# Optimization experiments

Hardware: AMD Instinct MI355X
Metric: run time of the kernel (lower is better)

Reference implementation:

```python
import jax, jax.numpy as jnp
import numpy as np

NC, ND = 100000, 100000
E, L = 500000, 100000
HID, OUT = 128, 64
NH, HD = 4, 32
NL = 2


def setup_inputs() -> dict:
    key = jax.random.key(0)
    ks = jax.random.split(key, 16)
    f = jnp.float32
    s_lin = 1.0 / np.sqrt(HID)
    s_rel = 1.0 / np.sqrt(HD)
    return {
        "emb_C": jax.random.normal(ks[0], (NC, HID), f) * 0.1,
        "emb_D": jax.random.normal(ks[1], (ND, HID), f) * 0.1,
        "kW": jax.random.normal(ks[2], (NL, 2, HID, HID), f) * s_lin,
        "kb": jnp.zeros((NL, 2, HID), f),
        "qW": jax.random.normal(ks[3], (NL, 2, HID, HID), f) * s_lin,
        "qb": jnp.zeros((NL, 2, HID), f),
        "vW": jax.random.normal(ks[4], (NL, 2, HID, HID), f) * s_lin,
        "vb": jnp.zeros((NL, 2, HID), f),
        "aW": jax.random.normal(ks[5], (NL, 2, HID, HID), f) * s_lin,
        "ab": jnp.zeros((NL, 2, HID), f),
        "skip": jnp.ones((NL, 2), f),
        "arel": jax.random.normal(ks[6], (NL, 2, NH, HD, HD), f) * s_rel,
        "mrel": jax.random.normal(ks[7], (NL, 2, NH, HD, HD), f) * s_rel,
        "prel": jnp.ones((NL, 2, NH), f),
        "outW": jax.random.normal(ks[8], (2, HID, OUT), f) * s_lin,
        "outb": jnp.zeros((2, OUT), f),
        # edge_index for (Compound -> Disease) and reverse (Disease -> Compound)
        "ei_cd": jnp.stack([jax.random.randint(ks[9], (E,), 0, NC),
                            jax.random.randint(ks[10], (E,), 0, ND)]).astype(jnp.int32),
        "ei_dc": jnp.stack([jax.random.randint(ks[11], (E,), 0, ND),
                            jax.random.randint(ks[12], (E,), 0, NC)]).astype(jnp.int32),
        # edge_label_index: (Compound, Disease) pairs to score
        "eli": jnp.stack([jax.random.randint(ks[13], (L,), 0, NC),
                          jax.random.randint(ks[14], (L,), 0, ND)]).astype(jnp.int32),
    }


def _seg_softmax(a, seg, n):
    # numerically stable softmax over edges grouped by destination node
    amax = jax.ops.segment_max(a, seg, num_segments=n)
    amax = jnp.where(jnp.isfinite(amax), amax, 0.0)
    ex = jnp.exp(a - amax[seg])
    den = jax.ops.segment_sum(ex, seg, num_segments=n)
    return ex / (den[seg] + 1e-16)


def _hgt_layer(xs, p, ei_cd, ei_dc):
    kW, kb, qW, qb, vW, vb, aW, ab, skip, arel, mrel, prel = p
    # per-node-type K/Q/V projections, reshaped to [N, heads, head_dim]
    k = [(xs[t] @ kW[t] + kb[t]).reshape(-1, NH, HD) for t in range(2)]
    q = [(xs[t] @ qW[t] + qb[t]).reshape(-1, NH, HD) for t in range(2)]
    v = [(xs[t] @ vW[t] + vb[t]).reshape(-1, NH, HD) for t in range(2)]
    outs = [jnp.zeros_like(k[0]), jnp.zeros_like(k[1])]
    rels = [(0, 1, ei_cd), (1, 0, ei_dc)]  # (src_type, dst_type, edge_index)
    for r, (s, d, ei) in enumerate(rels):
        # relation-specific transforms applied per source node (as in PyG HGTConv)
        krel = jnp.einsum('nhd,hde->nhe', k[s], arel[r])
        vrel = jnp.einsum('nhd,hde->nhe', v[s], mrel[r])
        src, dst = ei[0], ei[1]
        ndst = xs[d].shape[0]
        a = (q[d][dst] * krel[src]).sum(-1) * prel[r] / np.sqrt(HD)  # [E, NH]
        alpha = _seg_softmax(a, dst, ndst)
        msg = vrel[src] * alpha[..., None]                           # [E, NH, HD]
        outs[d] = outs[d] + jax.ops.segment_sum(msg, dst, num_segments=ndst)
    new = []
    for t in range(2):
        o = outs[t].reshape(-1, HID)
        o = jax.nn.gelu(o) @ aW[t] + ab[t]
        g = jax.nn.sigmoid(skip[t])
        new.append(g * o + (1.0 - g) * xs[t])  # skip connection (in==out dims)
    return new


def reference(emb_C, emb_D, kW, kb, qW, qb, vW, vb, aW, ab, skip, arel, mrel, prel,
              outW, outb, ei_cd, ei_dc, eli):
    xs = [emb_C, emb_D]
    for l in range(NL):
        p = (kW[l], kb[l], qW[l], qb[l], vW[l], vb[l], aW[l], ab[l],
             skip[l], arel[l], mrel[l], prel[l])
        xs = _hgt_layer(xs, p, ei_cd, ei_dc)
        xs = [jax.nn.relu(x) for x in xs]  # dropout(0.2) in eval mode -> identity
    zC = xs[0] @ outW[0] + outb[0]
    zD = xs[1] @ outW[1] + outb[1]
    logits = jnp.clip((zC[eli[0]] * zD[eli[1]]).sum(-1), -10.0, 10.0)
    return logits
```

## Files before the change

kernel.cpp:

```cpp
#include <hip/hip_runtime.h>
#include <math.h>

#define NC_   100000
#define ND_   100000
#define NN_   100000
#define E_CNT 500000
#define L_CNT 100000
#define NH_   4
#define HD_   32
#define WCAT_SZ (129 * 384)

typedef __attribute__((ext_vector_type(8))) short short8;
typedef __attribute__((ext_vector_type(4))) float floatx4;

__device__ __forceinline__ float gelu_f(float x) {
    const float c0 = 0.7978845608028654f;
    float x3 = x * x * x;
    return 0.5f * x * (1.0f + tanhf(c0 * (x + 0.044715f * x3)));
}

__device__ __forceinline__ unsigned short bf_rne(float x) {
    unsigned int u = __float_as_uint(x);
    u += 0x7fffu + ((u >> 16) & 1u);
    return (unsigned short)(u >> 16);
}
__device__ __forceinline__ float bf_to_f(unsigned short b) {
    return __uint_as_float(((unsigned int)b) << 16);
}

__global__ __launch_bounds__(256) void fill0_int(int* __restrict__ p, int n) {
    int i = blockIdx.x * 256 + threadIdx.x;
    if (i < n) p[i] = 0;
}

__global__ __launch_bounds__(256) void count_dst(const int* __restrict__ dstA,
                                                 const int* __restrict__ dstB,
                                                 int* __restrict__ cnt) {
    int r = blockIdx.y;
    const int* dst = r ? dstB : dstA;
    int e = blockIdx.x * 256 + threadIdx.x;
    if (e < E_CNT) atomicAdd(&cnt[r * NN_ + dst[e]], 1);
}

__global__ __launch_bounds__(256) void scan_a(const int* __restrict__ cnt,
                                              int* __restrict__ excl,
                                              int* __restrict__ partials) {
    __shared__ int sd[256];
    int r = blockIdx.y;
    cnt += r * NN_; excl += r * (NN_ + 1); partials += r * 128;
    int b = blockIdx.x, t = threadIdx.x;
    int base = b * 1024 + t * 4;
    int v0 = (base + 0 < NN_) ? cnt[base + 0] : 0;
    int v1 = (base + 1 < NN_) ? cnt[base + 1] : 0;
    int v2 = (base + 2 < NN_) ? cnt[base + 2] : 0;
    int v3 = (base + 3 < NN_) ? cnt[base + 3] : 0;
    int tsum = v0 + v1 + v2 + v3;
    sd[t] = tsum; __syncthreads();
    for (int off = 1; off < 256; off <<= 1) {
        int x = (t >= off) ? sd[t - off] : 0;
        __syncthreads();
        sd[t] += x;
        __syncthreads();
    }
    int excl_t = sd[t] - tsum;
    if (t == 255) partials[b] = sd[t];
    int q = excl_t;
    if (base + 0 < NN_) excl[base + 0] = q; q += v0;
    if (base + 1 < NN_) excl[base + 1] = q; q += v1;
    if (base + 2 < NN_) excl[base + 2] = q; q += v2;
    if (base + 3 < NN_) excl[base + 3] = q;
}

__global__ __launch_bounds__(128) void scan_b(int* __restrict__ partials) {
    __shared__ int sd[128];
    partials += blockIdx.x * 128;
    int t = threadIdx.x;
    int orig = (t < 98) ? partials[t] : 0;
    sd[t] = orig; __syncthreads();
    for (int off = 1; off < 128; off <<= 1) {
        int x = (t >= off) ? sd[t - off] : 0;
        __syncthreads();
        sd[t] += x;
        __syncthreads();
    }
    if (t < 98) partials[t] = sd[t] - orig;
}

__global__ __launch_bounds__(256) void scan_c(int* __restrict__ row_ptr,
                                              const int* __restrict__ partials,
                                              int* __restrict__ cursor) {
    int r = blockIdx.y;
    row_ptr += r * (NN_ + 1); partials += r * 128; cursor += r * NN_;
    int b = blockIdx.x, t = threadIdx.x;
    int base = b * 1024 + t * 4;
    int add = partials[b];
    #pragma unroll
    for (int j = 0; j < 4; j++) {
        int i = base + j;
        if (i < NN_) { int v = row_ptr[i] + add; row_ptr[i] = v; cursor[i] = v; }
    }
    if (b == 0 && t == 0) row_ptr[NN_] = E_CNT;
}

__global__ __launch_bounds__(256) void scatter_edges(const int* __restrict__ srcA,
                                                     const int* __restrict__ dstA,
                                                     const int* __restrict__ srcB,
                                                     const int* __restrict__ dstB,
                                                     int* __restrict__ cursor,
                                                     int* __restrict__ srcs) {
    int r = blockIdx.y;
    const int* src = r ? srcB : srcA;
    const int* dst = r ? dstB : dstA;
    cursor += r * NN_; srcs += r * E_CNT;
    int e = blockIdx.x * 256 + threadIdx.x;
    if (e >= E_CNT) return;
    int pos = atomicAdd(&cursor[dst[e]], 1);
    srcs[pos] = src[e];
}

__global__ void fuse_weights(const float* __restrict__ qW, const float* __restrict__ qb,
                             const float* __restrict__ kW, const float* __restrict__ kb,
                             const float* __restrict__ vW, const float* __restrict__ vb,
                             const float* __restrict__ arel, const float* __restrict__ mrel,
                             float* __restrict__ WcatAll)
{
    int i  = blockIdx.x;
    int t  = blockIdx.y;
    int lyr = blockIdx.z;
    int oc = threadIdx.x;
    int lt = lyr * 2 + t;
    float* Wcat = WcatAll + (size_t)lt * WCAT_SZ;
    float val;
    if (oc < 128) {
        val = (i < 128) ? qW[(size_t)(lt * 128 + i) * 128 + oc] : qb[lt * 128 + oc];
    } else {
        int which = (oc >= 256);
        int cc = oc - (which ? 256 : 128);
        int h = cc >> 5, e = cc & 31;
        const float* W = which ? vW : kW;
        const float* b = which ? vb : kb;
        const float* R = (which ? mrel : arel) + (size_t)(lt * NH_ + h) * HD_ * HD_ + e;
        float s = 0.f;
        if (i < 128) {
            const float* wrow = W + (size_t)(lt * 128 + i) * 128 + h * 32;
            #pragma unroll
            for (int d2 = 0; d2 < 32; d2++) s += wrow[d2] * R[d2 * 32];
        } else {
            const float* brow = b + lt * 128 + h * 32;
            #pragma unroll
            for (int d2 = 0; d2 < 32; d2++) s += brow[d2] * R[d2 * 32];
        }
        val = s;
    }
    Wcat[(size_t)((i < 128) ? i : 128) * 384 + oc] = val;
}

__global__ __launch_bounds__(128)
void split_w(const float* __restrict__ W, int ldw, int matStride,
             unsigned short* __restrict__ out, int N, int outMatStride)
{
    int n = blockIdx.x;
    int mat = blockIdx.y;
    int k = threadIdx.x;
    float x = W[(size_t)mat * matStride + (size_t)k * ldw + n];
    unsigned short b0 = bf_rne(x);
    float x1 = x - bf_to_f(b0);
    unsigned short b1 = bf_rne(x1);
    float x2 = x1 - bf_to_f(b1);
    unsigned short b2 = bf_rne(x2);
    int ps = N * 128;
    unsigned short* o = out + (size_t)mat * outMatStride + (size_t)n * 128 + k;
    o[0] = b0; o[ps] = b1; o[2 * ps] = b2;
}

template<int TN, int POST>
__global__ __launch_bounds__(256)
void gemm_mfma(const float* __restrict__ A, int lda,
               const unsigned short* __restrict__ Bs3, int pstride,
               const float* __restrict__ bias,
               float* __restrict__ C, int ldc, int M,
               const float* __restrict__ resid, const float* __restrict__ skipv,
               int ySplit,
               const float* __restrict__ A2, const unsigned short* __restrict__ Bs32,
               int pstride2, const float* __restrict__ bias2,
               float* __restrict__ C2, int ldc2)
{
    constexpr int CT = TN / 16;
    __shared__ unsigned short Asl[3 * 64 * 40];
    __shared__ unsigned short Bsl[3 * TN * 40];
    int by = blockIdx.y;
    if (ySplit >= 0 && by >= ySplit) {
        A = A2; Bs3 = Bs32; pstride = pstride2; bias = bias2; C = C2; ldc = ldc2;
        by -= ySplit;
    }
    int tid  = threadIdx.x;
    int wave = tid >> 6, lane = tid & 63;
    int quad = lane >> 4, l16 = lane & 15;
    int bm = blockIdx.x * 64;
    int bn = by * TN;

    floatx4 acc[CT];
    #pragma unroll
    for (int ct = 0; ct < CT; ct++) acc[ct] = (floatx4){0.f, 0.f, 0.f, 0.f};

    int sm = tid >> 2;
    int kq = (tid & 3) * 8;
    int arow = bm + sm;
    bool aval = arow < M;
    const float* ap = A + (size_t)arow * lda + kq;
    int sn = tid >> 1;
    int kh = (tid & 1) * 16;
    const unsigned short* bp = Bs3 + (size_t)(bn + sn) * 128 + kh;

    for (int ks = 0; ks < 128; ks += 32) {
        __syncthreads();
        float xv[8];
        if (aval) {
            *(float4*)&xv[0] = *(const float4*)(ap + ks);
            *(float4*)&xv[4] = *(const float4*)(ap + ks + 4);
        } else {
            #pragma unroll
            for (int i = 0; i < 8; i++) xv[i] = 0.f;
        }
        #pragma unroll
        for (int i = 0; i < 8; i += 2) {
            float xa = xv[i], xb = xv[i + 1];
            unsigned short a0 = bf_rne(xa); float ra = xa - bf_to_f(a0);
            unsigned short a1 = bf_rne(ra); float ra2 = ra - bf_to_f(a1);
            unsigned short a2 = bf_rne(ra2);
            unsigned short c0 = bf_rne(xb); float rb = xb - bf_to_f(c0);
            unsigned short c1 = bf_rne(rb); float rb2 = rb - bf_to_f(c1);
            unsigned short c2 = bf_rne(rb2);
            int idx = sm * 40 + kq + i;
            *(unsigned int*)&Asl[idx]            = (unsigned)a0 | ((unsigned)c0 << 16);
            *(unsigned int*)&Asl[2560 + idx]     = (unsigned)a1 | ((unsigned)c1 << 16);
            *(unsigned int*)&Asl[5120 + idx]     = (unsigned)a2 | ((unsigned)c2 << 16);
        }
        if (sn < TN) {
            #pragma unroll
            for (int p = 0; p < 3; p++) {
                uint4 v0 = *(const uint4*)(bp + (size_t)p * pstride + ks);
                uint4 v1 = *(const uint4*)(bp + (size_t)p * pstride + ks + 8);
                int bidx = p * (TN * 40) + sn * 40 + kh;
                *(uint4*)&Bsl[bidx]     = v0;
                *(uint4*)&Bsl[bidx + 8] = v1;
            }
        }
        __syncthreads();
        int am = wave * 16 + l16;
        short8 af0 = *(const short8*)&Asl[am * 40 + quad * 8];
        short8 af1 = *(const short8*)&Asl[2560 + am * 40 + quad * 8];
        short8 af2 = *(const short8*)&Asl[5120 + am * 40 + quad * 8];
        #pragma unroll
        for (int ct = 0; ct < CT; ct++) {
            int bnn = (ct * 16 + l16) * 40 + quad * 8;
            short8 bf0 = *(const short8*)&Bsl[bnn];
            short8 bf1 = *(const short8*)&Bsl[TN * 40 + bnn];
            short8 bf2 = *(const short8*)&Bsl[2 * TN * 40 + bnn];
            acc[ct] = __builtin_amdgcn_mfma_f32_16x16x32_bf16(af0, bf2, acc[ct], 0, 0, 0);
            acc[ct] = __builtin_amdgcn_mfma_f32_16x16x32_bf16(af1, bf1, acc[ct], 0, 0, 0);
            acc[ct] = __builtin_amdgcn_mfma_f32_16x16x32_bf16(af2, bf0, acc[ct], 0, 0, 0);
            acc[ct] = __builtin_amdgcn_mfma_f32_16x16x32_bf16(af0, bf1, acc[ct], 0, 0, 0);
            acc[ct] = __builtin_amdgcn_mfma_f32_16x16x32_bf16(af1, bf0, acc[ct], 0, 0, 0);
            acc[ct] = __builtin_amdgcn_mfma_f32_16x16x32_bf16(af0, bf0, acc[ct], 0, 0, 0);
        }
    }

    float g = 0.f, omg = 0.f;
    if (POST) { float sv = skipv[0]; g = 1.0f / (1.0f + expf(-sv)); omg = 1.0f - g; }
    #pragma unroll
    for (int ct = 0; ct < CT; ct++) {
        int col = bn + ct * 16 + l16;
        float bv = bias[col];
        #pragma unroll
        for (int i = 0; i < 4; i++) {
            int row = bm + wave * 16 + quad * 4 + i;
            if (row < M) {
                float v = acc[ct][i] + bv;
                if (POST) {
                    float r = resid[(size_t)row * ldc + col];
                    v = fmaxf(g * v + omg * r, 0.f);
                }
                C[(size_t)row * ldc + col] = v;
            }
        }
    }
}

__global__ __launch_bounds__(256)
void attn_gather(const int* __restrict__ row_ptr, const int* __restrict__ srcs,
                 float* __restrict__ qo, const float* __restrict__ kv,
                 const float* __restrict__ prel, int ndst)
{
    int wave = (blockIdx.x * 256 + threadIdx.x) >> 6;
    int lane = threadIdx.x & 63;
    if (wave >= ndst) return;
    int d = wave;
    int gl = lane & 15;
    int group = lane >> 4;
    int h = gl >> 2;
    float pr = prel[h] * 0.17677669529663687f;
    int beg = row_ptr[d], end = row_ptr[d + 1];
    const float* qrow = qo + (size_t)d * 128 + gl * 8;
    float4 q0 = *(const float4*)(qrow);
    float4 q1 = *(const float4*)(qrow + 4);
    float m = -1.0e30f, l = 0.f;
    float4 acc0 = make_float4(0.f,0.f,0.f,0.f), acc1 = acc0;
    int nt = (end - beg + 3) >> 2;
    for (int t = 0; t < nt; t++) {
        int i = beg + (t << 2) + group;
        if (i < end) {
            int s = srcs[i];
            const float* row = kv + (size_t)s * 256 + gl * 8;
            float4 k0 = *(const float4*)(row);
            float4 k1 = *(const float4*)(row + 4);
            float4 v0 = *(const float4*)(row + 128);
            float4 v1 = *(const float4*)(row + 132);
            float part = q0.x*k0.x + q0.y*k0.y + q0.z*k0.z + q0.w*k0.w
                       + q1.x*k1.x + q1.y*k1.y + q1.z*k1.z + q1.w*k1.w;
            part += __shfl_xor(part, 1);
            part += __shfl_xor(part, 2);
            float a = part * pr;
            float mn = fmaxf(m, a);
            float scale = expf(m - mn);
            float p = expf(a - mn);
            l = l * scale + p;
            acc0.x = acc0.x * scale + p * v0.x;
            acc0.y = acc0.y * scale + p * v0.y;
            acc0.z = acc0.z * scale + p * v0.z;
            acc0.w = acc0.w * scale + p * v0.w;
            acc1.x = acc1.x * scale + p * v1.x;
            acc1.y = acc1.y * scale + p * v1.y;
            acc1.z = acc1.z * scale + p * v1.z;
            acc1.w = acc1.w * scale + p * v1.w;
            m = mn;
        }
    }
    #pragma unroll
    for (int mask = 16; mask <= 32; mask <<= 1) {
        float m_o = __shfl_xor(m, mask);
        float l_o = __shfl_xor(l, mask);
        float4 a0o, a1o;
        a0o.x = __shfl_xor(acc0.x, mask); a0o.y = __shfl_xor(acc0.y, mask);
        a0o.z = __shfl_xor(acc0.z, mask); a0o.w = __shfl_xor(acc0.w, mask);
        a1o.x = __shfl_xor(acc1.x, mask); a1o.y = __shfl_xor(acc1.y, mask);
        a1o.z = __shfl_xor(acc1.z, mask); a1o.w = __shfl_xor(acc1.w, mask);
        float mn = fmaxf(m, m_o);
        float s0 = expf(m - mn), s1 = expf(m_o - mn);
        l = l * s0 + l_o * s1;
        acc0.x = acc0.x * s0 + a0o.x * s1; acc0.y = acc0.y * s0 + a0o.y * s1;
        acc0.z = acc0.z * s0 + a0o.z * s1; acc0.w = acc0.w * s0 + a0o.w * s1;
        acc1.x = acc1.x * s0 + a1o.x * s1; acc1.y = acc1.y * s0 + a1o.y * s1;
        acc1.z = acc1.z * s0 + a1o.z * s1; acc1.w = acc1.w * s0 + a1o.w * s1;
        m = mn;
    }
    float inv = (beg == end) ? 0.f : 1.f / (l + 1e-16f);
    if (group == 0) {
        float* orow = qo + (size_t)d * 128 + gl * 8;
        float4 o0, o1;
        o0.x = gelu_f(acc0.x * inv); o0.y = gelu_f(acc0.y * inv);
        o0.z = gelu_f(acc0.z * inv); o0.w = gelu_f(acc0.w * inv);
        o1.x = gelu_f(acc1.x * inv); o1.y = gelu_f(acc1.y * inv);
        o1.z = gelu_f(acc1.z * inv); o1.w = gelu_f(acc1.w * inv);
        *(float4*)(orow)     = o0;
        *(float4*)(orow + 4) = o1;
    }
}

__global__ __launch_bounds__(256)
void score_pairs(const int* __restrict__ ic, const int* __restrict__ id,
                 const float* __restrict__ zC, const float* __restrict__ zD,
                 float* __restrict__ out)
{
    int gid = blockIdx.x * 256 + threadIdx.x;
    int p = gid >> 4, lane = gid & 15;
    if (p >= L_CNT) return;
    int c = ic[p], d = id[p];
    float4 a = *(const float4*)(zC + (size_t)c * 64 + lane * 4);
    float4 b = *(const float4*)(zD + (size_t)d * 64 + lane * 4);
    float s = a.x * b.x + a.y * b.y + a.z * b.z + a.w * b.w;
    s += __shfl_down(s, 8, 16);
    s += __shfl_down(s, 4, 16);
    s += __shfl_down(s, 2, 16);
    s += __shfl_down(s, 1, 16);
    if (lane == 0) out[p] = fminf(10.0f, fmaxf(-10.0f, s));
}

extern "C" void kernel_launch(void* const* d_in, const int* in_sizes, int n_in,
                              void* d_out, int out_size, void* d_ws, size_t ws_size,
                              hipStream_t stream)
{
    float* xC = (float*)d_in[0];
    float* xD = (float*)d_in[1];
    const float* kW   = (const float*)d_in[2];
    const float* kb   = (const float*)d_in[3];
    const float* qW   = (const float*)d_in[4];
    const float* qb   = (const float*)d_in[5];
    const float* vW   = (const float*)d_in[6];
    const float* vb   = (const float*)d_in[7];
    const float* aW   = (const float*)d_in[8];
    const float* ab   = (const float*)d_in[9];
    const float* skip = (const float*)d_in[10];
    const float* arel = (const float*)d_in[11];
    const float* mrel = (const float*)d_in[12];
    const float* prel = (const float*)d_in[13];
    const float* outW = (const float*)d_in[14];
    const float* outb = (const float*)d_in[15];
    const int* ei_cd  = (const int*)d_in[16];
    const int* ei_dc  = (const int*)d_in[17];
    const int* eli    = (const int*)d_in[18];

    float* ws = (float*)d_ws;
    size_t off = 0;
    float* kv    = ws + off; off += (size_t)NN_ * 256;
    float* qo    = ws + off; off += (size_t)NN_ * 128;
    float* Wcat  = ws + off; off += (size_t)4 * WCAT_SZ;
    unsigned short* WsCat = (unsigned short*)(ws + off); off += (4 * 3 * 384 * 128) / 2;
    unsigned short* aWs   = (unsigned short*)(ws + off); off += (4 * 3 * 128 * 128) / 2;
    unsigned short* outWs = (unsigned short*)(ws + off); off += (2 * 3 * 64 * 128) / 2;
    int* iws = (int*)(ws + off);
    size_t ioff = 0;
    int* rp      = iws + ioff; ioff += 2 * (NN_ + 1);
    int* srcsA   = iws + ioff; ioff += 2 * E_CNT;
    int* cnt     = iws + ioff; ioff += 2 * NN_;
    int* cursor  = iws + ioff; ioff += 2 * NN_;
    int* partial = iws + ioff; ioff += 256;
    float* zC = kv;
    float* zD = kv + (size_t)NN_ * 128;

    const int gridM = (NN_ + 63) / 64;
    const int gE    = (E_CNT + 255) / 256;
    const int gN2   = (2 * NN_ + 255) / 256;
    const int gScan = 98;
    const int gGath = (NN_ + 3) / 4;

    fill0_int<<<gN2, 256, 0, stream>>>(cnt, 2 * NN_);
    count_dst<<<dim3(gE, 2), 256, 0, stream>>>(ei_cd + E_CNT, ei_dc + E_CNT, cnt);
    scan_a<<<dim3(gScan, 2), 256, 0, stream>>>(cnt, rp, partial);
    scan_b<<<2, 128, 0, stream>>>(partial);
    scan_c<<<dim3(gScan, 2), 256, 0, stream>>>(rp, partial, cursor);
    scatter_edges<<<dim3(gE, 2), 256, 0, stream>>>(ei_cd, ei_cd + E_CNT,
                                                   ei_dc, ei_dc + E_CNT, cursor, srcsA);
    int* rp_cd   = rp;
    int* rp_dc   = rp + (NN_ + 1);
    int* srcs_cd = srcsA;
    int* srcs_dc = srcsA + E_CNT;

    fuse_weights<<<dim3(129, 2, 2), 384, 0, stream>>>(qW, qb, kW, kb, vW, vb,
                                                      arel, mrel, Wcat);
    split_w<<<dim3(384, 4), 128, 0, stream>>>(Wcat, 384, WCAT_SZ, WsCat, 384, 3 * 384 * 128);
    split_w<<<dim3(128, 4), 128, 0, stream>>>(aW, 128, 128 * 128, aWs, 128, 3 * 128 * 128);
    split_w<<<dim3(64, 2), 128, 0, stream>>>(outW, 64, 128 * 64, outWs, 64, 3 * 64 * 128);

    const int PS_CAT = 384 * 128;
    const int PS_AW  = 128 * 128;
    const int PS_OW  = 64 * 128;

    for (int l = 0; l < 2; l++) {
        const float* abl = ab + (size_t)l * 2 * 128;
        float* WcC = Wcat + (size_t)(l * 2 + 0) * WCAT_SZ;
        float* WcD = Wcat + (size_t)(l * 2 + 1) * WCAT_SZ;
        const unsigned short* WsC = WsCat + (size_t)(l * 2 + 0) * 3 * PS_CAT;
        const unsigned short* WsD = WsCat + (size_t)(l * 2 + 1) * 3 * PS_CAT;
        const unsigned short* aWsD = aWs + (size_t)(l * 2 + 1) * 3 * PS_AW;
        const unsigned short* aWsC = aWs + (size_t)(l * 2 + 0) * 3 * PS_AW;

        gemm_mfma<128, 0><<<dim3(gridM, 3), 256, 0, stream>>>(
            xC, 128, WsC + 128 * 128, PS_CAT, WcC + 128 * 384 + 128, kv, 256, NC_,
            nullptr, nullptr,
            2, xD, WsD, PS_CAT, WcD + 128 * 384, qo, 128);
        attn_gather<<<gGath, 256, 0, stream>>>(rp_cd, srcs_cd, qo, kv,
                                               prel + (l * 2 + 0) * 4, ND_);

        gemm_mfma<128, 0><<<dim3(gridM, 2), 256, 0, stream>>>(
            xD, 128, WsD + 128 * 128, PS_CAT, WcD + 128 * 384 + 128, kv, 256, ND_,
            nullptr, nullptr, -1, nullptr, nullptr, 0, nullptr, nullptr, 0);

        gemm_mfma<128, 1><<<dim3(gridM, 1), 256, 0, stream>>>(
            qo, 128, aWsD, PS_AW, abl + 128, xD, 128, ND_,
            xD, skip + l * 2 + 1, -1, nullptr, nullptr, 0, nullptr, nullptr, 0);

        gemm_mfma<128, 0><<<dim3(gridM, 1), 256, 0, stream>>>(
            xC, 128, WsC, PS_CAT, WcC + 128 * 384, qo, 128, NC_,
            nullptr, nullptr, -1, nullptr, nullptr, 0, nullptr, nullptr, 0);
        attn_gather<<<gGath, 256, 0, stream>>>(rp_dc, srcs_dc, qo, kv,
                                               prel + (l * 2 + 1) * 4, NC_);

        gemm_mfma<128, 1><<<dim3(gridM, 1), 256, 0, stream>>>(
            qo, 128, aWsC, PS_AW, abl, xC, 128, NC_,
            xC, skip + l * 2 + 0, -1, nullptr, nullptr, 0, nullptr, nullptr, 0);
    }

    gemm_mfma<64, 0><<<dim3(gridM, 2), 256, 0, stream>>>(
        xC, 128, outWs, PS_OW, outb, zC, 64, NC_, nullptr, nullptr,
        1, xD, outWs + 3 * PS_OW, PS_OW, outb + 64, zD, 64);

    score_pairs<<<(L_CNT * 16 + 255) / 256, 256, 0, stream>>>(
        eli, eli + L_CNT, zC, zD, (float*)d_out);
}
```

Before: 1.278 ms.

## Pre-pack weights in MFMA fragment order and drop LDS staging in GEMM

New measurement: 1.301 ms. About the same (+1.9%).

```diff
diff --git a/kernel.cpp b/kernel.cpp
--- a/kernel.cpp
+++ b/kernel.cpp
@@ -155,42 +155,54 @@
     Wcat[(size_t)((i < 128) ? i : 128) * 384 + oc] = val;
 }
 
-__global__ __launch_bounds__(128)
-void split_w(const float* __restrict__ W, int ldw, int matStride,
-             unsigned short* __restrict__ out, int N, int outMatStride)
-{
-    int n = blockIdx.x;
+__global__ __launch_bounds__(256)
+void pack_w(const float* __restrict__ W, int ldw, int matStride,
+            unsigned short* __restrict__ out, int N, int outMatStride)
+{
     int mat = blockIdx.y;
-    int k = threadIdx.x;
-    float x = W[(size_t)mat * matStride + (size_t)k * ldw + n];
-    unsigned short b0 = bf_rne(x);
-    float x1 = x - bf_to_f(b0);
-    unsigned short b1 = bf_rne(x1);
-    float x2 = x1 - bf_to_f(b1);
-    unsigned short b2 = bf_rne(x2);
+    int e = blockIdx.x * 256 + threadIdx.x;
+    int total = N * 16;
+    if (e >= total) return;
+    int lane = e & 63;
+    int s = (e >> 6) & 3;
+    int nt = e >> 8;
+    int col = nt * 16 + (lane & 15);
+    int k0 = s * 32 + ((lane >> 4) << 3);
+    const float* src = W + (size_t)mat * matStride + (size_t)k0 * ldw + col;
     int ps = N * 128;
-    unsigned short* o = out + (size_t)mat * outMatStride + (size_t)n * 128 + k;
-    o[0] = b0; o[ps] = b1; o[2 * ps] = b2;
+    unsigned short* o = out + (size_t)mat * outMatStride + (size_t)e * 8;
+    short8 p0, p1, p2;
+    #pragma unroll
+    for (int j = 0; j < 8; j++) {
+        float x = src[(size_t)j * ldw];
+        unsigned short b0 = bf_rne(x);
+        float x1 = x - bf_to_f(b0);
+        unsigned short b1 = bf_rne(x1);
+        float x2 = x1 - bf_to_f(b1);
+        unsigned short b2 = bf_rne(x2);
+        p0[j] = (short)b0; p1[j] = (short)b1; p2[j] = (short)b2;
+    }
+    *(short8*)(o)          = p0;
+    *(short8*)(o + ps)     = p1;
+    *(short8*)(o + 2 * ps) = p2;
 }
 
 template<int TN, int POST>
-__global__ __launch_bounds__(256)
+__global__ __launch_bounds__(256, 4)
 void gemm_mfma(const float* __restrict__ A, int lda,
-               const unsigned short* __restrict__ Bs3, int pstride,
+               const unsigned short* __restrict__ Bp, int pstride,
                const float* __restrict__ bias,
                float* __restrict__ C, int ldc, int M,
                const float* __restrict__ resid, const float* __restrict__ skipv,
                int ySplit,
-               const float* __restrict__ A2, const unsigned short* __restrict__ Bs32,
+               const float* __restrict__ A2, const unsigned short* __restrict__ Bp2,
                int pstride2, const float* __restrict__ bias2,
                float* __restrict__ C2, int ldc2)
 {
     constexpr int CT = TN / 16;
-    __shared__ unsigned short Asl[3 * 64 * 40];
-    __shared__ unsigned short Bsl[3 * TN * 40];
     int by = blockIdx.y;
     if (ySplit >= 0 && by >= ySplit) {
-        A = A2; Bs3 = Bs32; pstride = pstride2; bias = bias2; C = C2; ldc = ldc2;
+        A = A2; Bp = Bp2; pstride = pstride2; bias = bias2; C = C2; ldc = ldc2;
         by -= ySplit;
     }
     int tid  = threadIdx.x;
@@ -199,70 +211,47 @@
     int bm = blockIdx.x * 64;
     int bn = by * TN;
 
+    int row = bm + wave * 16 + l16;
+    bool rv = row < M;
+    const float* ap = A + (size_t)row * lda + quad * 8;
+    const unsigned short* bp = Bp + (size_t)(bn >> 4) * 2048 + (size_t)lane * 8;
+
     floatx4 acc[CT];
     #pragma unroll
     for (int ct = 0; ct < CT; ct++) acc[ct] = (floatx4){0.f, 0.f, 0.f, 0.f};
 
-    int sm = tid >> 2;
-    int kq = (tid & 3) * 8;
-    int arow = bm + sm;
-    bool aval = arow < M;
-    const float* ap = A + (size_t)arow * lda + kq;
-    int sn = tid >> 1;
-    int kh = (tid & 1) * 16;
-    const unsigned short* bp = Bs3 + (size_t)(bn + sn) * 128 + kh;
-
-    for (int ks = 0; ks < 128; ks += 32) {
-        __syncthreads();
+    for (int s = 0; s < 4; s++) {
         float xv[8];
-        if (aval) {
-            *(float4*)&xv[0] = *(const float4*)(ap + ks);
-            *(float4*)&xv[4] = *(const float4*)(ap + ks + 4);
+        if (rv) {
+            *(float4*)&xv[0] = *(const float4*)(ap + s * 32);
+            *(float4*)&xv[4] = *(const float4*)(ap + s * 32 + 4);
         } else {
             #pragma unroll
             for (int i = 0; i < 8; i++) xv[i] = 0.f;
         }
+        short8 af0, af1, af2;
         #pragma unroll
-        for (int i = 0; i < 8; i += 2) {
-            float xa = xv[i], xb = xv[i + 1];
-            unsigned short a0 = bf_rne(xa); float ra = xa - bf_to_f(a0);
-            unsigned short a1 = bf_rne(ra); float ra2 = ra - bf_to_f(a1);
-            unsigned short a2 = bf_rne(ra2);
-            unsigned short c0 = bf_rne(xb); float rb = xb - bf_to_f(c0);
-            unsigned short c1 = bf_rne(rb); float rb2 = rb - bf_to_f(c1);
-            unsigned short c2 = bf_rne(rb2);
-            int idx = sm * 40 + kq + i;
-            *(unsigned int*)&Asl[idx]            = (unsigned)a0 | ((unsigned)c0 << 16);
-            *(unsigned int*)&Asl[2560 + idx]     = (unsigned)a1 | ((unsigned)c1 << 16);
-            *(unsigned int*)&Asl[5120 + idx]     = (unsigned)a2 | ((unsigned)c2 << 16);
-        }
-        if (sn < TN) {
-            #pragma unroll
-            for (int p = 0; p < 3; p++) {
-                uint4 v0 = *(const uint4*)(bp + (size_t)p * pstride + ks);
-                uint4 v1 = *(const uint4*)(bp + (size_t)p * pstride + ks + 8);
-                int bidx = p * (TN * 40) + sn * 40 + kh;
-                *(uint4*)&Bsl[bidx]     = v0;
-                *(uint4*)&Bsl[bidx + 8] = v1;
-            }
-        }
-        __syncthreads();
-        int am = wave * 16 + l16;
-        short8 af0 = *(const short8*)&Asl[am * 40 + quad * 8];
-        short8 af1 = *(const short8*)&Asl[2560 + am * 40 + quad * 8];
-        short8 af2 = *(const short8*)&Asl[5120 + am * 40 + quad * 8];
+        for (int i = 0; i < 8; i++) {
+            float x = xv[i];
+            unsigned short b0 = bf_rne(x);
+            float x1 = x - bf_to_f(b0);
+            unsigned short b1 = bf_rne(x1);
+            float x2 = x1 - bf_to_f(b1);
+            unsigned short b2 = bf_rne(x2);
+            af0[i] = (short)b0; af1[i] = (short)b1; af2[i] = (short)b2;
+        }
         #pragma unroll
         for (int ct = 0; ct < CT; ct++) {
-            int bnn = (ct * 16 + l16) * 40 + quad * 8;
-            short8 bf0 = *(const short8*)&Bsl[bnn];
-            short8 bf1 = *(const short8*)&Bsl[TN * 40 + bnn];
-            short8 bf2 = *(const short8*)&Bsl[2 * TN * 40 + bnn];
-            acc[ct] = __builtin_amdgcn_mfma_f32_16x16x32_bf16(af0, bf2, acc[ct], 0, 0, 0);
-            acc[ct] = __builtin_amdgcn_mfma_f32_16x16x32_bf16(af1, bf1, acc[ct], 0, 0, 0);
-            acc[ct] = __builtin_amdgcn_mfma_f32_16x16x32_bf16(af2, bf0, acc[ct], 0, 0, 0);
-            acc[ct] = __builtin_amdgcn_mfma_f32_16x16x32_bf16(af0, bf1, acc[ct], 0, 0, 0);
-            acc[ct] = __builtin_amdgcn_mfma_f32_16x16x32_bf16(af1, bf0, acc[ct], 0, 0, 0);
-            acc[ct] = __builtin_amdgcn_mfma_f32_16x16x32_bf16(af0, bf0, acc[ct], 0, 0, 0);
+            const unsigned short* bf = bp + (size_t)ct * 2048 + s * 512;
+            short8 b0 = *(const short8*)(bf);
+            short8 b1 = *(const short8*)(bf + pstride);
+            short8 b2 = *(const short8*)(bf + 2 * (size_t)pstride);
+            acc[ct] = __builtin_amdgcn_mfma_f32_16x16x32_bf16(af0, b2, acc[ct], 0, 0, 0);
+            acc[ct] = __builtin_amdgcn_mfma_f32_16x16x32_bf16(af1, b1, acc[ct], 0, 0, 0);
+            acc[ct] = __builtin_amdgcn_mfma_f32_16x16x32_bf16(af2, b0, acc[ct], 0, 0, 0);
+            acc[ct] = __builtin_amdgcn_mfma_f32_16x16x32_bf16(af0, b1, acc[ct], 0, 0, 0);
+            acc[ct] = __builtin_amdgcn_mfma_f32_16x16x32_bf16(af1, b0, acc[ct], 0, 0, 0);
+            acc[ct] = __builtin_amdgcn_mfma_f32_16x16x32_bf16(af0, b0, acc[ct], 0, 0, 0);
         }
     }
 
@@ -274,14 +263,14 @@
         float bv = bias[col];
         #pragma unroll
         for (int i = 0; i < 4; i++) {
-            int row = bm + wave * 16 + quad * 4 + i;
-            if (row < M) {
+            int r = bm + wave * 16 + quad * 4 + i;
+            if (r < M) {
                 float v = acc[ct][i] + bv;
                 if (POST) {
-                    float r = resid[(size_t)row * ldc + col];
-                    v = fmaxf(g * v + omg * r, 0.f);
+                    float rr = resid[(size_t)r * ldc + col];
+                    v = fmaxf(g * v + omg * rr, 0.f);
                 }
-                C[(size_t)row * ldc + col] = v;
+                C[(size_t)r * ldc + col] = v;
             }
         }
     }
@@ -448,9 +437,12 @@
 
     fuse_weights<<<dim3(129, 2, 2), 384, 0, stream>>>(qW, qb, kW, kb, vW, vb,
                                                       arel, mrel, Wcat);
-    split_w<<<dim3(384, 4), 128, 0, stream>>>(Wcat, 384, WCAT_SZ, WsCat, 384, 3 * 384 * 128);
-    split_w<<<dim3(128, 4), 128, 0, stream>>>(aW, 128, 128 * 128, aWs, 128, 3 * 128 * 128);
-    split_w<<<dim3(64, 2), 128, 0, stream>>>(outW, 64, 128 * 64, outWs, 64, 3 * 64 * 128);
+    pack_w<<<dim3((384 * 16 + 255) / 256, 4), 256, 0, stream>>>(
+        Wcat, 384, WCAT_SZ, WsCat, 384, 3 * 384 * 128);
+    pack_w<<<dim3((128 * 16 + 255) / 256, 4), 256, 0, stream>>>(
+        aW, 128, 128 * 128, aWs, 128, 3 * 128 * 128);
+    pack_w<<<dim3((64 * 16 + 255) / 256, 2), 256, 0, stream>>>(
+        outW, 64, 128 * 64, outWs, 64, 3 * 64 * 128);
 
     const int PS_CAT = 384 * 128;
     const int PS_AW  = 128 * 128;
```
